# Kernel optimization log

Measured on AMD Instinct MI355X. Metric: run time of the kernel, lower is better.

## Reference

```python
import jax, jax.numpy as jnp
import numpy as np

NUM_HEADS = 12
HEAD_DIM = 128
DIM = NUM_HEADS * HEAD_DIM  # 1536
FRAMES = 8
GRID_H, GRID_W = 15, 26
SPATIAL = GRID_H * GRID_W  # 390
SEQ = FRAMES * SPATIAL      # 3120
EPS = 1e-5


def setup_inputs() -> dict:
    key = jax.random.key(0)
    ks = jax.random.split(key, 12)
    w = lambda k, shape, s=0.02: jax.random.normal(k, shape, dtype=jnp.float32) * s
    return {
        "x": jax.random.normal(ks[0], (1, SEQ, DIM), dtype=jnp.float32),
        "freqs": jax.random.uniform(ks[1], (SEQ, HEAD_DIM // 2), dtype=jnp.float32) * 6.283,
        "Wq": w(ks[2], (DIM, DIM)), "bq": jnp.zeros((DIM,), jnp.float32), "gq": jnp.ones((DIM,), jnp.float32),
        "Wk": w(ks[3], (DIM, DIM)), "bk": jnp.zeros((DIM,), jnp.float32), "gk": jnp.ones((DIM,), jnp.float32),
        "Wv": w(ks[4], (DIM, DIM)), "bv": jnp.zeros((DIM,), jnp.float32),
        "Wo": w(ks[5], (DIM, DIM)), "bo": jnp.zeros((DIM,), jnp.float32),
        "qk_frame_bias": w(ks[6], (FRAMES, DIM), 0.05),
        "v_frame_bias": w(ks[7], (FRAMES, DIM), 0.05),
        "v_spatial_bias": w(ks[8], (SPATIAL, DIM), 0.05),
    }


def _rmsnorm(x, g):
    return x * jax.lax.rsqrt(jnp.mean(x * x, axis=-1, keepdims=True) + EPS) * g


def _rope(x, freqs):
    # x: [b, s, dim] -> per-head interleaved complex rotation (Wan-style)
    b, s, _ = x.shape
    xp = x.reshape(b, s, NUM_HEADS, HEAD_DIM // 2, 2)
    cos = jnp.cos(freqs)[None, :, None, :]  # [1, s, 1, d/2]
    sin = jnp.sin(freqs)[None, :, None, :]
    xr, xi = xp[..., 0], xp[..., 1]
    out = jnp.stack([xr * cos - xi * sin, xr * sin + xi * cos], axis=-1)
    return out.reshape(b, s, DIM)


def _expand_frame(bias):
    # [FRAMES, dim] -> [1, FRAMES*SPATIAL, dim] (each frame vector repeated over spatial tokens)
    return jnp.broadcast_to(bias[:, None, :], (FRAMES, SPATIAL, DIM)).reshape(1, SEQ, DIM)


def _expand_spatial(bias):
    # [SPATIAL, dim] -> [1, FRAMES*SPATIAL, dim] (tiled over frames)
    return jnp.broadcast_to(bias[None, :, :], (FRAMES, SPATIAL, DIM)).reshape(1, SEQ, DIM)


def reference(x, freqs, Wq, bq, gq, Wk, bk, gk, Wv, bv, Wo, bo,
              qk_frame_bias, v_frame_bias, v_spatial_bias):
    q = _rmsnorm(x @ Wq + bq, gq)
    k = _rmsnorm(x @ Wk + bk, gk)
    v = x @ Wv + bv
    q = _rope(q, freqs)
    k = _rope(k, freqs)
    qk_bias = _expand_frame(qk_frame_bias)
    q = q + qk_bias
    k = k + qk_bias
    v = v + _expand_frame(v_frame_bias) + _expand_spatial(v_spatial_bias)
    b, s, _ = x.shape
    qh = q.reshape(b, s, NUM_HEADS, HEAD_DIM)
    kh = k.reshape(b, s, NUM_HEADS, HEAD_DIM)
    vh = v.reshape(b, s, NUM_HEADS, HEAD_DIM)
    scale = 1.0 / np.sqrt(HEAD_DIM)
    scores = jnp.einsum("bqnd,bknd->bnqk", qh, kh) * scale
    attn = jax.nn.softmax(scores, axis=-1)
    out = jnp.einsum("bnqk,bknd->bqnd", attn, vh).reshape(b, s, DIM)
    return out @ Wo + bo
```

## Files before the change

kernel.cpp:

```cpp
#include <hip/hip_runtime.h>
#include <cstdint>

#define SEQ     3120
#define SPAD    3200
#define DIM     1536
#define NQKV    4608
#define HEADS   12
#define HD      128
#define SPATIAL 390
#define EPSV    1e-5f
#define KVBLK   64
#define NTILES  49
#define NEGBIG  (-1e30f)
#define QSCALE  (0.08838834764831845f * 1.4426950408889634f)
#define CROW(r, hi) ((((r) & 3) + 8 * ((r) >> 2)) + 4 * (hi))

typedef unsigned short u16;
typedef short s16x8 __attribute__((ext_vector_type(8)));
typedef float f32x4 __attribute__((ext_vector_type(4)));
typedef float f32x16 __attribute__((ext_vector_type(16)));

__device__ __forceinline__ u16 f2bf(float f) {
  union { float f; unsigned u; } v; v.f = f;
  unsigned r = v.u + 0x7FFFu + ((v.u >> 16) & 1u);
  return (u16)(r >> 16);
}
__device__ __forceinline__ float bf2f(u16 b) {
  union { unsigned u; float f; } v; v.u = ((unsigned)b) << 16;
  return v.f;
}
__device__ __forceinline__ unsigned cvtpk(float lo, float hi) {
  unsigned r;
  asm("v_cvt_pk_bf16_f32 %0, %1, %2" : "=v"(r) : "v"(lo), "v"(hi));
  return r;
}
__device__ __forceinline__ void gload16(const void* g, const void* l) {
  __builtin_amdgcn_global_load_lds(
      (const __attribute__((address_space(1))) unsigned*)g,
      (__attribute__((address_space(3))) unsigned*)(uintptr_t)l,
      16, 0, 0);
}

__global__ __launch_bounds__(256) void k_convert_x(
    const float* __restrict__ x, const float* __restrict__ bq,
    const float* __restrict__ bk, const float* __restrict__ bv,
    u16* __restrict__ xb, float* __restrict__ bcat) {
  if (blockIdx.x == 0) {
    for (int j = threadIdx.x; j < NQKV; j += 256)
      bcat[j] = (j < DIM) ? bq[j] : (j < 2 * DIM) ? bk[j - DIM] : bv[j - 2 * DIM];
  }
  const int i = (blockIdx.x * 256 + threadIdx.x) * 4;
  if (i >= SPAD * DIM) return;
  const int row = i / DIM;
  float4 v = make_float4(0.f, 0.f, 0.f, 0.f);
  if (row < SEQ) v = *(const float4*)(x + i);
  const unsigned lo = (unsigned)f2bf(v.x) | ((unsigned)f2bf(v.y) << 16);
  const unsigned hi = (unsigned)f2bf(v.z) | ((unsigned)f2bf(v.w) << 16);
  *(uint2*)(xb + i) = make_uint2(lo, hi);
}

__global__ __launch_bounds__(256) void k_transpose_w(
    const float* __restrict__ Wq, const float* __restrict__ Wk,
    const float* __restrict__ Wv, const float* __restrict__ Wo,
    u16* __restrict__ WtAll, u16* __restrict__ WoT) {
  const int wsel = blockIdx.z;
  const float* W = (wsel == 0) ? Wq : (wsel == 1) ? Wk : (wsel == 2) ? Wv : Wo;
  __shared__ float t[64][65];
  const int k0 = blockIdx.x * 64, n0 = blockIdx.y * 64;
  const int c = threadIdx.x & 63, r4 = threadIdx.x >> 6;
#pragma unroll
  for (int rr = 0; rr < 64; rr += 4)
    t[r4 + rr][c] = W[(size_t)(k0 + r4 + rr) * DIM + n0 + c];
  __syncthreads();
  u16* Wt = (wsel < 3) ? (WtAll + (size_t)wsel * DIM * DIM) : WoT;
  const int kp = threadIdx.x & 31;
  const int r8 = threadIdx.x >> 5;
#pragma unroll
  for (int rr = 0; rr < 64; rr += 8) {
    const int n = r8 + rr;
    const unsigned v = (unsigned)f2bf(t[2 * kp][n]) |
                       ((unsigned)f2bf(t[2 * kp + 1][n]) << 16);
    *(unsigned*)&Wt[(size_t)(n0 + n) * DIM + k0 + 2 * kp] = v;
  }
}

template <int OUT_BF16>
__global__ __launch_bounds__(256) void k_gemm(const u16* __restrict__ A,
                                              const u16* __restrict__ Bt,
                                              const float* __restrict__ bias,
                                              void* __restrict__ Cout,
                                              int N, int K, int storeMmax,
                                              int nbx) {
  __shared__ short As[8192];
  __shared__ short Bs[8192];
  const int nwg = gridDim.x;
  const int q = nwg >> 3, r = nwg & 7;
  const int xcd = blockIdx.x & 7, idx = blockIdx.x >> 3;
  const int swz = (xcd < r ? xcd * (q + 1) : r * (q + 1) + (xcd - r) * q) + idx;
  const int bxi = swz % nbx, byi = swz / nbx;
  const int brow = byi * 128, bcol = bxi * 128;

  const int tid = threadIdx.x;
  const int lane = tid & 63, wv = tid >> 6;
  const int l15 = lane & 15, g = lane >> 4;
  const int wr = wv >> 1, wc = wv & 1;

  const f32x4 z4 = {0.f, 0.f, 0.f, 0.f};
  f32x4 acc[4][4];
#pragma unroll
  for (int m = 0; m < 4; ++m)
#pragma unroll
    for (int n = 0; n < 4; ++n) acc[m][n] = z4;

  const u16* Ap[4];
  const u16* Bp[4];
  const int sch = ((lane & 7) ^ ((lane >> 3) & 7)) * 8;
#pragma unroll
  for (int it = 0; it < 4; ++it) {
    const int row = it * 32 + wv * 8 + (lane >> 3);
    Ap[it] = A + (size_t)(brow + row) * K + sch;
    Bp[it] = Bt + (size_t)(bcol + row) * K + sch;
  }

  for (int k0 = 0; k0 < K; k0 += 64) {
    __syncthreads();
#pragma unroll
    for (int it = 0; it < 4; ++it) {
      gload16(Ap[it] + k0, As + (it * 32 + wv * 8) * 64);
      gload16(Bp[it] + k0, Bs + (it * 32 + wv * 8) * 64);
    }
    __syncthreads();
#pragma unroll
    for (int kk = 0; kk < 2; ++kk) {
      s16x8 a[4], b[4];
#pragma unroll
      for (int m = 0; m < 4; ++m)
        a[m] = *(const s16x8*)&As[(wr * 64 + m * 16 + l15) * 64 +
                                  (((kk * 4 + g) ^ (l15 & 7)) * 8)];
#pragma unroll
      for (int n = 0; n < 4; ++n)
        b[n] = *(const s16x8*)&Bs[(wc * 64 + n * 16 + l15) * 64 +
                                  (((kk * 4 + g) ^ (l15 & 7)) * 8)];
#pragma unroll
      for (int m = 0; m < 4; ++m)
#pragma unroll
        for (int n = 0; n < 4; ++n)
          acc[m][n] = __builtin_amdgcn_mfma_f32_16x16x32_bf16(a[m], b[n], acc[m][n], 0, 0, 0);
    }
  }

#pragma unroll
  for (int m = 0; m < 4; ++m) {
#pragma unroll
    for (int n = 0; n < 4; ++n) {
      const int cc = bcol + wc * 64 + n * 16 + l15;
      const float bb = bias[cc];
#pragma unroll
      for (int i = 0; i < 4; ++i) {
        const int rr = brow + wr * 64 + m * 16 + g * 4 + i;
        if (rr < storeMmax) {
          const float v = acc[m][n][i] + bb;
          if (OUT_BF16) ((u16*)Cout)[(size_t)rr * N + cc] = f2bf(v);
          else          ((float*)Cout)[(size_t)rr * N + cc] = v;
        }
      }
    }
  }
}

__global__ __launch_bounds__(256) void k_post(
    const u16* __restrict__ Pqkv, const float* __restrict__ freqs,
    const float* __restrict__ gq, const float* __restrict__ gk,
    const float* __restrict__ qkfb, const float* __restrict__ vfb,
    const float* __restrict__ vsb,
    u16* __restrict__ Qf, u16* __restrict__ Kf, u16* __restrict__ Vf) {
  const int s = blockIdx.x;
  const int t = threadIdx.x;
  const int fidx = s / SPATIAL;
  const int sp = s - fidx * SPATIAL;
  __shared__ float cs[64], sn[64];
  __shared__ float red[8];
  if (t < 64) {
    const float a = freqs[s * 64 + t];
    cs[t] = __cosf(a);
    sn[t] = __sinf(a);
  }
  const u16* qrow = Pqkv + (size_t)s * NQKV;
  const u16* krow = qrow + DIM;
  const u16* vrow = qrow + 2 * DIM;
  s16x8 q8, k8, v8;
  float sq = 0.f, sk = 0.f;
  if (t < 192) {
    q8 = *(const s16x8*)(qrow + 8 * t);
    k8 = *(const s16x8*)(krow + 8 * t);
    v8 = *(const s16x8*)(vrow + 8 * t);
#pragma unroll
    for (int i = 0; i < 8; ++i) {
      const float a = bf2f((u16)q8[i]); sq += a * a;
      const float b = bf2f((u16)k8[i]); sk += b * b;
    }
  }
#pragma unroll
  for (int off = 1; off < 64; off <<= 1) {
    sq += __shfl_xor(sq, off);
    sk += __shfl_xor(sk, off);
  }
  const int lane = t & 63, wv = t >> 6;
  if (lane == 0) { red[wv] = sq; red[wv + 4] = sk; }
  __syncthreads();
  sq = red[0] + red[1] + red[2] + red[3];
  sk = red[4] + red[5] + red[6] + red[7];
  const float rq = rsqrtf(sq * (1.0f / DIM) + EPSV);
  const float rk = rsqrtf(sk * (1.0f / DIM) + EPSV);
  if (t >= 192) return;
  const int d0 = 8 * t;
  float GQ[8], GK[8], FB[8], VF[8], VS[8];
  *(float4*)&GQ[0] = *(const float4*)(gq + d0);
  *(float4*)&GQ[4] = *(const float4*)(gq + d0 + 4);
  *(float4*)&GK[0] = *(const float4*)(gk + d0);
  *(float4*)&GK[4] = *(const float4*)(gk + d0 + 4);
  *(float4*)&FB[0] = *(const float4*)(qkfb + fidx * DIM + d0);
  *(float4*)&FB[4] = *(const float4*)(qkfb + fidx * DIM + d0 + 4);
  *(float4*)&VF[0] = *(const float4*)(vfb + fidx * DIM + d0);
  *(float4*)&VF[4] = *(const float4*)(vfb + fidx * DIM + d0 + 4);
  *(float4*)&VS[0] = *(const float4*)(vsb + (size_t)sp * DIM + d0);
  *(float4*)&VS[4] = *(const float4*)(vsb + (size_t)sp * DIM + d0 + 4);
  unsigned qo[4], ko[4], vo[4];
#pragma unroll
  for (int pi = 0; pi < 4; ++pi) {
    const int pin = (4 * t + pi) & 63;
    const float c = cs[pin], s_ = sn[pin];
    float xr = bf2f((u16)q8[2 * pi]) * rq * GQ[2 * pi];
    float xi = bf2f((u16)q8[2 * pi + 1]) * rq * GQ[2 * pi + 1];
    const float q0 = (xr * c - xi * s_ + FB[2 * pi]) * QSCALE;
    const float q1 = (xr * s_ + xi * c + FB[2 * pi + 1]) * QSCALE;
    qo[pi] = (unsigned)f2bf(q0) | ((unsigned)f2bf(q1) << 16);
    xr = bf2f((u16)k8[2 * pi]) * rk * GK[2 * pi];
    xi = bf2f((u16)k8[2 * pi + 1]) * rk * GK[2 * pi + 1];
    const float kk0 = xr * c - xi * s_ + FB[2 * pi];
    const float kk1 = xr * s_ + xi * c + FB[2 * pi + 1];
    ko[pi] = (unsigned)f2bf(kk0) | ((unsigned)f2bf(kk1) << 16);
    const float v0 = bf2f((u16)v8[2 * pi]) + VF[2 * pi] + VS[2 * pi];
    const float v1 = bf2f((u16)v8[2 * pi + 1]) + VF[2 * pi + 1] + VS[2 * pi + 1];
    vo[pi] = (unsigned)f2bf(v0) | ((unsigned)f2bf(v1) << 16);
  }
  *(uint4*)(Qf + (size_t)s * DIM + d0) = make_uint4(qo[0], qo[1], qo[2], qo[3]);
  *(uint4*)(Kf + (size_t)s * DIM + d0) = make_uint4(ko[0], ko[1], ko[2], ko[3]);
  *(uint4*)(Vf + (size_t)s * DIM + d0) = make_uint4(vo[0], vo[1], vo[2], vo[3]);
}

__global__ __launch_bounds__(256) void k_transpose_v(const u16* __restrict__ Vf,
                                                     u16* __restrict__ Vt) {
  __shared__ u16 tile[64][65];
  const int s0 = blockIdx.x * 64, c0 = blockIdx.y * 64;
  const int c = threadIdx.x & 63, r4 = threadIdx.x >> 6;
#pragma unroll
  for (int rr = 0; rr < 64; rr += 4) {
    const int s = s0 + r4 + rr;
    tile[r4 + rr][c] = (s < SEQ) ? Vf[(size_t)s * DIM + c0 + c] : (u16)0;
  }
  __syncthreads();
#pragma unroll
  for (int rr = 0; rr < 64; rr += 4) {
    const int dglob = c0 + r4 + rr;
    Vt[(size_t)dglob * SPAD + s0 + c] = tile[c][r4 + rr];
  }
}

__global__ __launch_bounds__(320, 2) void k_attn(const u16* __restrict__ Qf,
                                                 const u16* __restrict__ Kf,
                                                 const u16* __restrict__ Vt,
                                                 u16* __restrict__ AttO) {
  __shared__ short Ks[2][8192];
  __shared__ short Vs[2][8192];
  const int bid = blockIdx.x;
  const int gb = (bid & 7) * 30 + (bid >> 3);
  const int h = gb / 20;
  const int bx = gb - h * 20;
  const int tid = threadIdx.x;
  const int lane = tid & 63, w = tid >> 6;
  const int l31 = lane & 31, hi = lane >> 5;
  const int qrow = bx * 160 + w * 32 + l31;

  s16x8 qb[8];
  {
    const u16* qp = Qf + (size_t)qrow * DIM + h * HD + hi * 8;
#pragma unroll
    for (int s = 0; s < 8; ++s) qb[s] = *(const s16x8*)(qp + s * 16);
  }

  f32x16 o[4];
#pragma unroll
  for (int d = 0; d < 4; ++d)
#pragma unroll
    for (int r = 0; r < 16; ++r) o[d][r] = 0.f;
  float sl = 0.f;

  const u16* Kp[4];
  const u16* Vp[4];
  if (w < 4) {
#pragma unroll
    for (int it = 0; it < 4; ++it) {
      const int krow = w * 16 + it * 4 + (lane >> 4);
      const int kch = (lane & 15) ^ (it * 4 + (lane >> 4));
      Kp[it] = Kf + (size_t)krow * DIM + h * HD + kch * 8;
      const int vrow = w * 32 + it * 8 + (lane >> 3);
      const int vch = (lane & 7) ^ (lane >> 3);
      Vp[it] = Vt + (size_t)(h * HD + vrow) * SPAD + vch * 8;
    }
  }
  auto stage = [&](int T, int B) {
    const size_t kof = (size_t)T * KVBLK * DIM;
    const int vof = T * KVBLK;
#pragma unroll
    for (int it = 0; it < 4; ++it) {
      gload16(Kp[it] + kof, &Ks[B][(w * 16 + it * 4) * 128]);
      gload16(Vp[it] + vof, &Vs[B][(w * 32 + it * 8) * 64]);
    }
  };

  if (w < 4) {
    asm volatile("s_waitcnt vmcnt(0)" ::: "memory");
    stage(0, 0);
  }

  for (int t = 0; t < NTILES; ++t) {
    const int b = t & 1;
    if (w < 4) {
      if (t + 1 < NTILES) {
        stage(t + 1, b ^ 1);
        asm volatile("s_waitcnt vmcnt(8)" ::: "memory");
      } else {
        asm volatile("s_waitcnt vmcnt(0)" ::: "memory");
      }
    }
    __builtin_amdgcn_s_barrier();
    __builtin_amdgcn_sched_barrier(0);

    f32x16 st[2];
#pragma unroll
    for (int r = 0; r < 16; ++r) { st[0][r] = 0.f; st[1][r] = 0.f; }
    __builtin_amdgcn_s_setprio(1);
#pragma unroll
    for (int grp = 0; grp < 2; ++grp)
#pragma unroll
      for (int s = 0; s < 8; ++s) {
        const s16x8 ka = *(const s16x8*)&Ks[b][(grp * 32 + l31) * 128 +
                                              (((2 * s + hi) ^ (lane & 15)) * 8)];
        st[grp] = __builtin_amdgcn_mfma_f32_32x32x16_bf16(ka, qb[s], st[grp], 0, 0, 0);
      }
    __builtin_amdgcn_s_setprio(0);

    s16x8 vb[4][4];
#pragma unroll
    for (int s = 0; s < 4; ++s)
#pragma unroll
      for (int d = 0; d < 4; ++d)
        vb[s][d] = *(const s16x8*)&Vs[b][(d * 32 + l31) * 64 +
                                         (((2 * s + hi) ^ (lane & 7)) * 8)];

    if (t == NTILES - 1) {
#pragma unroll
      for (int r = 8; r < 16; ++r) st[1][r] = NEGBIG;
    }
    unsigned W[16], X[16];
    float p0s = 0.f, p1s = 0.f, p2s = 0.f, p3s = 0.f;
#pragma unroll
    for (int grp = 0; grp < 2; ++grp)
#pragma unroll
      for (int i = 0; i < 8; ++i) {
        const float p0 = exp2f(st[grp][2 * i]);
        const float p1 = exp2f(st[grp][2 * i + 1]);
        if (grp) { p2s += p0; p3s += p1; } else { p0s += p0; p1s += p1; }
        W[grp * 8 + i] = cvtpk(p0, p1);
      }
    sl += (p0s + p1s) + (p2s + p3s);
#pragma unroll
    for (int j = 0; j < 16; ++j) X[j] = __shfl_xor((int)W[j], 32);

    __builtin_amdgcn_s_setprio(1);
#pragma unroll
    for (int s = 0; s < 4; ++s) {
      const int base = (s >> 1) * 8 + (s & 1) * 4;
      unsigned pw[4];
      pw[0] = hi ? X[base + 2] : W[base + 0];
      pw[1] = hi ? X[base + 3] : W[base + 1];
      pw[2] = hi ? W[base + 2] : X[base + 0];
      pw[3] = hi ? W[base + 3] : X[base + 1];
      const s16x8 pa = *(const s16x8*)pw;
#pragma unroll
      for (int d = 0; d < 4; ++d)
        o[d] = __builtin_amdgcn_mfma_f32_32x32x16_bf16(pa, vb[s][d], o[d], 0, 0, 0);
    }
    __builtin_amdgcn_s_setprio(0);
    __builtin_amdgcn_s_barrier();
    __builtin_amdgcn_sched_barrier(0);
  }

  sl += __shfl_xor(sl, 32);
  const float rs = 1.0f / sl;
#pragma unroll
  for (int r = 0; r < 16; ++r) {
    const float rq = __shfl(rs, CROW(r, hi));
    const int row = bx * 160 + w * 32 + CROW(r, hi);
    if (row < SEQ) {
#pragma unroll
      for (int d = 0; d < 4; ++d)
        AttO[(size_t)row * DIM + h * HD + d * 32 + l31] = f2bf(o[d][r] * rq);
    }
  }
}

extern "C" void kernel_launch(void* const* d_in, const int* in_sizes, int n_in,
                              void* d_out, int out_size, void* d_ws, size_t ws_size,
                              hipStream_t stream) {
  const float* x    = (const float*)d_in[0];
  const float* freqs= (const float*)d_in[1];
  const float* Wq   = (const float*)d_in[2];
  const float* bq   = (const float*)d_in[3];
  const float* gq   = (const float*)d_in[4];
  const float* Wk   = (const float*)d_in[5];
  const float* bk   = (const float*)d_in[6];
  const float* gk   = (const float*)d_in[7];
  const float* Wv   = (const float*)d_in[8];
  const float* bv   = (const float*)d_in[9];
  const float* Wo   = (const float*)d_in[10];
  const float* bo   = (const float*)d_in[11];
  const float* qkfb = (const float*)d_in[12];
  const float* vfb  = (const float*)d_in[13];
  const float* vsb  = (const float*)d_in[14];

  if (ws_size < (size_t)87705600) return;

  char* ws = (char*)d_ws;
  u16*   xb    = (u16*)(ws);
  u16*   Vt    = (u16*)(ws);
  u16*   WtAll = (u16*)(ws + 9830400);
  u16*   WoT   = (u16*)(ws + 23986176);
  float* bcat  = (float*)(ws + 28704768);
  u16*   Pqkv  = (u16*)(ws + 28723200);
  u16*   AttO  = (u16*)(ws + 28723200);
  u16*   Qf    = (u16*)(ws + 58214400);
  u16*   Kf    = (u16*)(ws + 68044800);
  u16*   Vf    = (u16*)(ws + 77875200);

  k_convert_x<<<4800, 256, 0, stream>>>(x, bq, bk, bv, xb, bcat);
  k_transpose_w<<<dim3(24, 24, 4), 256, 0, stream>>>(Wq, Wk, Wv, Wo, WtAll, WoT);
  k_gemm<1><<<900, 256, 0, stream>>>(xb, WtAll, bcat, Pqkv, NQKV, DIM, SPAD, 36);
  k_post<<<SEQ, 256, 0, stream>>>(Pqkv, freqs, gq, gk, qkfb, vfb, vsb, Qf, Kf, Vf);
  k_transpose_v<<<dim3(50, 24), 256, 0, stream>>>(Vf, Vt);
  k_attn<<<240, 320, 0, stream>>>(Qf, Kf, Vt, AttO);
  k_gemm<0><<<300, 256, 0, stream>>>(AttO, WoT, bo, d_out, DIM, DIM, SEQ, 12);
}
```

Baseline: 255.2 us.

## Double-buffer GEMM LDS loads and merge x-convert with weight transpose

The GEMM main loop now uses two LDS buffers and issues the global-to-LDS loads for the next K tile before computing the current one. It waits with an explicit vmcnt count rather than two full syncthreads per iteration, so memory latency can overlap the MFMA work. Separately, the x bf16 conversion and the weight transpose kernels are merged into one launch to remove a kernel boundary. Doubling LDS to 64KB per block may lower occupancy.

```diff
diff --git a/kernel.cpp b/kernel.cpp
--- a/kernel.cpp
+++ b/kernel.cpp
@@ -41,46 +41,50 @@
       16, 0, 0);
 }
 
-__global__ __launch_bounds__(256) void k_convert_x(
+__global__ __launch_bounds__(256) void k_prep(
     const float* __restrict__ x, const float* __restrict__ bq,
     const float* __restrict__ bk, const float* __restrict__ bv,
-    u16* __restrict__ xb, float* __restrict__ bcat) {
-  if (blockIdx.x == 0) {
-    for (int j = threadIdx.x; j < NQKV; j += 256)
-      bcat[j] = (j < DIM) ? bq[j] : (j < 2 * DIM) ? bk[j - DIM] : bv[j - 2 * DIM];
-  }
-  const int i = (blockIdx.x * 256 + threadIdx.x) * 4;
-  if (i >= SPAD * DIM) return;
-  const int row = i / DIM;
-  float4 v = make_float4(0.f, 0.f, 0.f, 0.f);
-  if (row < SEQ) v = *(const float4*)(x + i);
-  const unsigned lo = (unsigned)f2bf(v.x) | ((unsigned)f2bf(v.y) << 16);
-  const unsigned hi = (unsigned)f2bf(v.z) | ((unsigned)f2bf(v.w) << 16);
-  *(uint2*)(xb + i) = make_uint2(lo, hi);
-}
-
-__global__ __launch_bounds__(256) void k_transpose_w(
     const float* __restrict__ Wq, const float* __restrict__ Wk,
     const float* __restrict__ Wv, const float* __restrict__ Wo,
+    u16* __restrict__ xb, float* __restrict__ bcat,
     u16* __restrict__ WtAll, u16* __restrict__ WoT) {
-  const int wsel = blockIdx.z;
-  const float* W = (wsel == 0) ? Wq : (wsel == 1) ? Wk : (wsel == 2) ? Wv : Wo;
   __shared__ float t[64][65];
-  const int k0 = blockIdx.x * 64, n0 = blockIdx.y * 64;
-  const int c = threadIdx.x & 63, r4 = threadIdx.x >> 6;
-#pragma unroll
-  for (int rr = 0; rr < 64; rr += 4)
-    t[r4 + rr][c] = W[(size_t)(k0 + r4 + rr) * DIM + n0 + c];
-  __syncthreads();
-  u16* Wt = (wsel < 3) ? (WtAll + (size_t)wsel * DIM * DIM) : WoT;
-  const int kp = threadIdx.x & 31;
-  const int r8 = threadIdx.x >> 5;
-#pragma unroll
-  for (int rr = 0; rr < 64; rr += 8) {
-    const int n = r8 + rr;
-    const unsigned v = (unsigned)f2bf(t[2 * kp][n]) |
-                       ((unsigned)f2bf(t[2 * kp + 1][n]) << 16);
-    *(unsigned*)&Wt[(size_t)(n0 + n) * DIM + k0 + 2 * kp] = v;
+  const int bid = blockIdx.x;
+  if (bid < 4800) {
+    if (bid == 0) {
+      for (int j = threadIdx.x; j < NQKV; j += 256)
+        bcat[j] = (j < DIM) ? bq[j] : (j < 2 * DIM) ? bk[j - DIM] : bv[j - 2 * DIM];
+    }
+    const int i = (bid * 256 + threadIdx.x) * 4;
+    if (i >= SPAD * DIM) return;
+    const int row = i / DIM;
+    float4 v = make_float4(0.f, 0.f, 0.f, 0.f);
+    if (row < SEQ) v = *(const float4*)(x + i);
+    const unsigned lo = (unsigned)f2bf(v.x) | ((unsigned)f2bf(v.y) << 16);
+    const unsigned hi = (unsigned)f2bf(v.z) | ((unsigned)f2bf(v.w) << 16);
+    *(uint2*)(xb + i) = make_uint2(lo, hi);
+  } else {
+    const int tb = bid - 4800;
+    const int wsel = tb / 576;
+    const int rem = tb - wsel * 576;
+    const int byi = rem / 24, bxi = rem - (rem / 24) * 24;
+    const float* W = (wsel == 0) ? Wq : (wsel == 1) ? Wk : (wsel == 2) ? Wv : Wo;
+    const int k0 = bxi * 64, n0 = byi * 64;
+    const int c = threadIdx.x & 63, r4 = threadIdx.x >> 6;
+#pragma unroll
+    for (int rr = 0; rr < 64; rr += 4)
+      t[r4 + rr][c] = W[(size_t)(k0 + r4 + rr) * DIM + n0 + c];
+    __syncthreads();
+    u16* Wt = (wsel < 3) ? (WtAll + (size_t)wsel * DIM * DIM) : WoT;
+    const int kp = threadIdx.x & 31;
+    const int r8 = threadIdx.x >> 5;
+#pragma unroll
+    for (int rr = 0; rr < 64; rr += 8) {
+      const int n = r8 + rr;
+      const unsigned v = (unsigned)f2bf(t[2 * kp][n]) |
+                         ((unsigned)f2bf(t[2 * kp + 1][n]) << 16);
+      *(unsigned*)&Wt[(size_t)(n0 + n) * DIM + k0 + 2 * kp] = v;
+    }
   }
 }
 
@@ -91,8 +95,8 @@
                                               void* __restrict__ Cout,
                                               int N, int K, int storeMmax,
                                               int nbx) {
-  __shared__ short As[8192];
-  __shared__ short Bs[8192];
+  __shared__ short As[2][8192];
+  __shared__ short Bs[2][8192];
   const int nwg = gridDim.x;
   const int q = nwg >> 3, r = nwg & 7;
   const int xcd = blockIdx.x & 7, idx = blockIdx.x >> 3;
@@ -121,32 +125,47 @@
     Ap[it] = A + (size_t)(brow + row) * K + sch;
     Bp[it] = Bt + (size_t)(bcol + row) * K + sch;
   }
-
-  for (int k0 = 0; k0 < K; k0 += 64) {
-    __syncthreads();
+  auto stage = [&](int T, int B) {
+    const int k0 = T * 64;
 #pragma unroll
     for (int it = 0; it < 4; ++it) {
-      gload16(Ap[it] + k0, As + (it * 32 + wv * 8) * 64);
-      gload16(Bp[it] + k0, Bs + (it * 32 + wv * 8) * 64);
-    }
-    __syncthreads();
+      gload16(Ap[it] + k0, &As[B][(it * 32 + wv * 8) * 64]);
+      gload16(Bp[it] + k0, &Bs[B][(it * 32 + wv * 8) * 64]);
+    }
+  };
+
+  const int NK = K >> 6;
+  stage(0, 0);
+
+  for (int t = 0; t < NK; ++t) {
+    const int b = t & 1;
+    if (t + 1 < NK) {
+      stage(t + 1, b ^ 1);
+      asm volatile("s_waitcnt vmcnt(8)" ::: "memory");
+    } else {
+      asm volatile("s_waitcnt vmcnt(0)" ::: "memory");
+    }
+    __builtin_amdgcn_s_barrier();
+    __builtin_amdgcn_sched_barrier(0);
 #pragma unroll
     for (int kk = 0; kk < 2; ++kk) {
-      s16x8 a[4], b[4];
+      s16x8 a[4], bfr[4];
 #pragma unroll
       for (int m = 0; m < 4; ++m)
-        a[m] = *(const s16x8*)&As[(wr * 64 + m * 16 + l15) * 64 +
-                                  (((kk * 4 + g) ^ (l15 & 7)) * 8)];
+        a[m] = *(const s16x8*)&As[b][(wr * 64 + m * 16 + l15) * 64 +
+                                     (((kk * 4 + g) ^ (l15 & 7)) * 8)];
 #pragma unroll
       for (int n = 0; n < 4; ++n)
-        b[n] = *(const s16x8*)&Bs[(wc * 64 + n * 16 + l15) * 64 +
-                                  (((kk * 4 + g) ^ (l15 & 7)) * 8)];
+        bfr[n] = *(const s16x8*)&Bs[b][(wc * 64 + n * 16 + l15) * 64 +
+                                       (((kk * 4 + g) ^ (l15 & 7)) * 8)];
 #pragma unroll
       for (int m = 0; m < 4; ++m)
 #pragma unroll
         for (int n = 0; n < 4; ++n)
-          acc[m][n] = __builtin_amdgcn_mfma_f32_16x16x32_bf16(a[m], b[n], acc[m][n], 0, 0, 0);
-    }
+          acc[m][n] = __builtin_amdgcn_mfma_f32_16x16x32_bf16(a[m], bfr[n], acc[m][n], 0, 0, 0);
+    }
+    __builtin_amdgcn_s_barrier();
+    __builtin_amdgcn_sched_barrier(0);
   }
 
 #pragma unroll
@@ -444,8 +463,8 @@
   u16*   Kf    = (u16*)(ws + 68044800);
   u16*   Vf    = (u16*)(ws + 77875200);
 
-  k_convert_x<<<4800, 256, 0, stream>>>(x, bq, bk, bv, xb, bcat);
-  k_transpose_w<<<dim3(24, 24, 4), 256, 0, stream>>>(Wq, Wk, Wv, Wo, WtAll, WoT);
+  k_prep<<<7104, 256, 0, stream>>>(x, bq, bk, bv, Wq, Wk, Wv, Wo,
+                                   xb, bcat, WtAll, WoT);
   k_gemm<1><<<900, 256, 0, stream>>>(xb, WtAll, bcat, Pqkv, NQKV, DIM, SPAD, 36);
   k_post<<<SEQ, 256, 0, stream>>>(Pqkv, freqs, gq, gk, qkfb, vfb, vsb, Qf, Kf, Vf);
   k_transpose_v<<<dim3(50, 24), 256, 0, stream>>>(Vf, Vt);
```

Result: faster. 245.6 us (-3.8%).
